# Optimization experiments

Measured on AMD Instinct MI355X. Metric: run time of the kernel, lower is better.

## Reference

```python
import jax, jax.numpy as jnp
import numpy as np

# -------- static config (mirrors init_kwargs / buffers at init) --------
B, S, H = 4, 2048, 1024
CTX, E, K = 64, 8, 2
POS_D = CTX // 2                 # 32
DG = H + CTX + POS_D             # 1120 actual gate-input width
HID = 3072                       # ByteMLP: 256*ceil(int(2*(4*DG)/3)/256)
N = B * S
# capacity = min(max(int(ceil(N*1.25/E) * mean(1/(clamp(0.5)+0.1))), 4), 2048)
CAPACITY = 2048
AUX_COEF = 0.01


def rmsnorm(x, w, eps=1e-6):
    return x * jax.lax.rsqrt(jnp.mean(x * x, axis=-1, keepdims=True) + eps) * w


def setup_inputs() -> dict:
    key = jax.random.key(0)
    ks = jax.random.split(key, 10)
    p = lambda k, shp: jax.random.normal(k, shp, jnp.float32) * 0.02
    return {
        "x": jax.random.normal(ks[0], (B, S, H), jnp.float32),
        "positions": jax.random.randint(ks[1], (B, S), 0, 4096, jnp.int32),
        "w_c1": p(ks[2], (H, 2 * H)), "b_c1": jnp.zeros((2 * H,), jnp.float32),
        "w_c2": p(ks[3], (2 * H, CTX)), "b_c2": jnp.zeros((CTX,), jnp.float32),
        "norm_w": jnp.ones((DG,), jnp.float32),
        "mlp_w1": p(ks[4], (DG, HID)),
        "mlp_w3": p(ks[5], (DG, HID)),
        "mlp_w2": p(ks[6], (HID, DG)),
        "proj_w": p(ks[7], (DG, E)),
        "pos_table": p(ks[8], (4096, POS_D)),
        "temperature": jnp.float32(1.0),
    }


def _gate(x, positions, w_c1, b_c1, w_c2, b_c2, norm_w, mlp_w1, mlp_w2, mlp_w3,
          proj_w, pos_table, temperature):
    x_flat = x.reshape(N, H)
    pos_emb = pos_table[positions.reshape(-1)]                       # [N,32]
    ctx = jax.nn.gelu(x_flat @ w_c1 + b_c1, approximate=False) @ w_c2 + b_c2
    context_feat = jnp.concatenate([ctx, pos_emb], axis=-1)          # [N,96]
    gi = jnp.concatenate([x_flat, context_feat], axis=-1)            # [N,DG]
    gi = rmsnorm(gi, norm_w)
    h = (jax.nn.silu(gi @ mlp_w1) * (gi @ mlp_w3)) @ mlp_w2          # SwiGLU MLP
    h = h + gi                                                       # residual
    logits = h @ proj_w                                              # [N,E]
    # expert_priority buffer == ones -> log prior is 0 (omitted)
    # expert_load buffer == zeros -> load_imbalance == 0 -> temp = temperature
    temp = jnp.maximum(temperature, 0.3)
    return jax.nn.softmax(logits / temp, axis=-1), context_feat


def reference(x, positions, w_c1, b_c1, w_c2, b_c2, norm_w, mlp_w1, mlp_w2,
              mlp_w3, proj_w, pos_table, temperature):
    scores, context_feat = _gate(x, positions, w_c1, b_c1, w_c2, b_c2, norm_w,
                                 mlp_w1, mlp_w2, mlp_w3, proj_w, pos_table,
                                 temperature)
    topk_scores, topk_idx = jax.lax.top_k(scores, K)                 # [N,K]

    # ---- vectorized greedy capacity dispatch (== torch per-token loop) ----
    fe = topk_idx.reshape(-1)                                        # [N*K]
    fw = topk_scores.reshape(-1)                                     # priority==1
    order = jnp.argsort(-fw)                                         # desc by weight
    e_sorted = fe[order]
    oh = jax.nn.one_hot(e_sorted, E, dtype=jnp.int32)                # [N*K,E]
    rank = jnp.take_along_axis(jnp.cumsum(oh, 0), e_sorted[:, None], 1)[:, 0] - 1
    ok = rank < CAPACITY
    slot_sorted = jnp.where(ok, rank, -1)
    NK = N * K
    slot = jnp.zeros((NK,), jnp.int32).at[order].set(slot_sorted.astype(jnp.int32))
    assigned = jnp.zeros((NK,), bool).at[order].set(ok)
    assigned_mask = assigned.reshape(N, K)
    buffer_positions = jnp.maximum(slot, 0).reshape(N, K)
    overflow_mask = ~assigned_mask.any(axis=-1)
    expert_count = jax.ops.segment_sum(assigned.astype(jnp.int32), fe,
                                       num_segments=E)

    # ---- load-balance aux loss (switch-style) ----
    me = scores.mean(axis=0)                                         # mean prob/expert
    ce = expert_count.astype(scores.dtype) / N                       # assigned frac
    aux_loss = AUX_COEF * E * jnp.sum(me * ce)

    next_context = context_feat.reshape(B, S, -1).mean(axis=1)       # [B,96]
    return (topk_idx, topk_scores, assigned_mask, buffer_positions,
            overflow_mask, expert_count, aux_loss, next_context)
```

## Files before the change

### kernel.cpp

```cpp
#include <hip/hip_runtime.h>
#include <math.h>

#define N_TOK 8192
#define HD    1024
#define CTXD  64
#define POS_D 32
#define DG    1120
#define HID   3072
#define NE    8
#define CAP   2048
#define NK    (N_TOK * 2)
#define CH    2048

typedef _Float16 half8 __attribute__((ext_vector_type(8)));
typedef float    floatx4 __attribute__((ext_vector_type(4)));

__device__ static inline void gl2lds16(const void* g, void* l) {
  __builtin_amdgcn_global_load_lds(
      (const __attribute__((address_space(1))) void*)g,
      (__attribute__((address_space(3))) void*)l, 16, 0, 0);
}

__global__ __launch_bounds__(256) void mfma_gemm(
    const _Float16* __restrict__ Ah, const _Float16* __restrict__ Al, int lda,
    const _Float16* __restrict__ Bh, const _Float16* __restrict__ Bl, int ldb,
    int Bn,
    const float* __restrict__ bias,
    float* __restrict__ Cf, _Float16* __restrict__ Oh, _Float16* __restrict__ Ol,
    int ldc,
    int Kd, int mode)
{
  __shared__ _Float16 smem[16384];
  _Float16* sAh = smem;
  _Float16* sAl = smem + 4096;
  _Float16* sBh = smem + 8192;
  _Float16* sBl = smem + 12288;

  const int tid = threadIdx.x;
  const int m0 = blockIdx.y * 128, n0 = blockIdx.x * 128;
  const int kbeg = blockIdx.z * Kd;

  const int q0 = tid, q1 = tid + 256;
  const int r0 = q0 >> 2, r1 = q1 >> 2;
  const int cg0 = (q0 & 3) ^ ((r0 >> 1) & 3);
  const int cg1 = (q1 & 3) ^ ((r1 >> 1) & 3);
  int br0 = n0 + r0; if (br0 >= Bn) br0 = Bn - 1;
  int br1 = n0 + r1; if (br1 >= Bn) br1 = Bn - 1;
  const _Float16* gA0h = Ah + (size_t)(m0 + r0) * lda + kbeg + cg0 * 8;
  const _Float16* gA1h = Ah + (size_t)(m0 + r1) * lda + kbeg + cg1 * 8;
  const _Float16* gA0l = Al + (size_t)(m0 + r0) * lda + kbeg + cg0 * 8;
  const _Float16* gA1l = Al + (size_t)(m0 + r1) * lda + kbeg + cg1 * 8;
  const _Float16* gB0h = Bh + (size_t)br0 * ldb + kbeg + cg0 * 8;
  const _Float16* gB1h = Bh + (size_t)br1 * ldb + kbeg + cg1 * 8;
  const _Float16* gB0l = Bl + (size_t)br0 * ldb + kbeg + cg0 * 8;
  const _Float16* gB1l = Bl + (size_t)br1 * ldb + kbeg + cg1 * 8;

  const int lane = tid & 63;
  const int wave = tid >> 6;
  const int wm = (wave >> 1) * 64, wn = (wave & 1) * 64;
  const int fr = lane & 15, quad = lane >> 4;
  int aoff[4], boff[4];
#pragma unroll
  for (int t = 0; t < 4; ++t) {
    int ar = wm + t * 16 + fr;
    aoff[t] = ar * 32 + (quad ^ ((ar >> 1) & 3)) * 8;
    int brr = wn + t * 16 + fr;
    boff[t] = brr * 32 + (quad ^ ((brr >> 1) & 3)) * 8;
  }

  floatx4 acc[4][4];
#pragma unroll
  for (int i = 0; i < 4; ++i)
#pragma unroll
    for (int j = 0; j < 4; ++j) {
      floatx4 z = {0.f, 0.f, 0.f, 0.f};
      acc[i][j] = z;
    }

  for (int k0 = 0; k0 < Kd; k0 += 32) {
    gl2lds16(gA0h, sAh + q0 * 8);
    gl2lds16(gA1h, sAh + q1 * 8);
    gl2lds16(gA0l, sAl + q0 * 8);
    gl2lds16(gA1l, sAl + q1 * 8);
    gl2lds16(gB0h, sBh + q0 * 8);
    gl2lds16(gB1h, sBh + q1 * 8);
    gl2lds16(gB0l, sBl + q0 * 8);
    gl2lds16(gB1l, sBl + q1 * 8);
    gA0h += 32; gA1h += 32; gA0l += 32; gA1l += 32;
    gB0h += 32; gB1h += 32; gB0l += 32; gB1l += 32;
    __syncthreads();

    half8 a_h[4], a_l[4], b_h[4], b_l[4];
#pragma unroll
    for (int t = 0; t < 4; ++t) {
      a_h[t] = *(const half8*)(sAh + aoff[t]);
      a_l[t] = *(const half8*)(sAl + aoff[t]);
      b_h[t] = *(const half8*)(sBh + boff[t]);
      b_l[t] = *(const half8*)(sBl + boff[t]);
    }
#pragma unroll
    for (int i = 0; i < 4; ++i)
#pragma unroll
      for (int j = 0; j < 4; ++j) {
        acc[i][j] = __builtin_amdgcn_mfma_f32_16x16x32_f16(a_h[i], b_h[j], acc[i][j], 0, 0, 0);
        acc[i][j] = __builtin_amdgcn_mfma_f32_16x16x32_f16(a_h[i], b_l[j], acc[i][j], 0, 0, 0);
        acc[i][j] = __builtin_amdgcn_mfma_f32_16x16x32_f16(a_l[i], b_h[j], acc[i][j], 0, 0, 0);
      }
    __syncthreads();
  }

#pragma unroll
  for (int j = 0; j < 4; ++j) {
    int col = n0 + wn + j * 16 + fr;
    if (col < Bn) {
      float bv = bias ? bias[col] : 0.f;
#pragma unroll
      for (int i = 0; i < 4; ++i) {
#pragma unroll
        for (int r = 0; r < 4; ++r) {
          int row = m0 + wm + i * 16 + quad * 4 + r;
          size_t idx = (size_t)row * ldc + col;
          float v = acc[i][j][r] + bv;
          if (mode == 1) {
            v = 0.5f * v * (1.0f + erff(v * 0.70710678118654752440f));
            _Float16 hh = (_Float16)v;
            Oh[idx] = hh; Ol[idx] = (_Float16)(v - (float)hh);
          } else if (mode == 5) {
            atomicAdd(&Cf[idx], v);
          } else {
            Cf[idx] = v;
          }
        }
      }
    }
  }
}

__global__ __launch_bounds__(256, 3) void mfma_swiglu64(
    const _Float16* __restrict__ Ah, const _Float16* __restrict__ Al, int lda,
    const _Float16* __restrict__ B1h, const _Float16* __restrict__ B1l,
    const _Float16* __restrict__ B2h, const _Float16* __restrict__ B2l, int ldb,
    _Float16* __restrict__ Oh, _Float16* __restrict__ Ol, int ldc,
    int Kd)
{
  __shared__ _Float16 smem[16384];
  _Float16* sAh  = smem;
  _Float16* sAl  = smem + 4096;
  _Float16* sB1h = smem + 8192;
  _Float16* sB1l = smem + 10240;
  _Float16* sB2h = smem + 12288;
  _Float16* sB2l = smem + 14336;

  const int tid = threadIdx.x;
  const int m0 = blockIdx.y * 128, n0 = blockIdx.x * 64;

  const int q0 = tid, q1 = tid + 256;
  const int ra0 = q0 >> 2, ra1 = q1 >> 2;
  const int ca0 = (q0 & 3) ^ ((ra0 >> 1) & 3);
  const int ca1 = (q1 & 3) ^ ((ra1 >> 1) & 3);
  const _Float16* gA0h = Ah + (size_t)(m0 + ra0) * lda + ca0 * 8;
  const _Float16* gA1h = Ah + (size_t)(m0 + ra1) * lda + ca1 * 8;
  const _Float16* gA0l = Al + (size_t)(m0 + ra0) * lda + ca0 * 8;
  const _Float16* gA1l = Al + (size_t)(m0 + ra1) * lda + ca1 * 8;
  const int rb = tid >> 2;
  const int cb = (tid & 3) ^ ((rb >> 1) & 3);
  const _Float16* gB1hp = B1h + (size_t)(n0 + rb) * ldb + cb * 8;
  const _Float16* gB1lp = B1l + (size_t)(n0 + rb) * ldb + cb * 8;
  const _Float16* gB2hp = B2h + (size_t)(n0 + rb) * ldb + cb * 8;
  const _Float16* gB2lp = B2l + (size_t)(n0 + rb) * ldb + cb * 8;

  const int lane = tid & 63;
  const int wave = tid >> 6;
  const int wm = (wave >> 1) * 64, wn = (wave & 1) * 32;
  const int fr = lane & 15, quad = lane >> 4;
  int aoff[4], boff[2];
#pragma unroll
  for (int t = 0; t < 4; ++t) {
    int ar = wm + t * 16 + fr;
    aoff[t] = ar * 32 + (quad ^ ((ar >> 1) & 3)) * 8;
  }
#pragma unroll
  for (int t = 0; t < 2; ++t) {
    int brr = wn + t * 16 + fr;
    boff[t] = brr * 32 + (quad ^ ((brr >> 1) & 3)) * 8;
  }

  floatx4 acc1[4][2], acc2[4][2];
#pragma unroll
  for (int i = 0; i < 4; ++i)
#pragma unroll
    for (int j = 0; j < 2; ++j) {
      floatx4 z = {0.f, 0.f, 0.f, 0.f};
      acc1[i][j] = z; acc2[i][j] = z;
    }

  for (int k0 = 0; k0 < Kd; k0 += 32) {
    gl2lds16(gA0h, sAh + q0 * 8);
    gl2lds16(gA1h, sAh + q1 * 8);
    gl2lds16(gA0l, sAl + q0 * 8);
    gl2lds16(gA1l, sAl + q1 * 8);
    gl2lds16(gB1hp, sB1h + tid * 8);
    gl2lds16(gB1lp, sB1l + tid * 8);
    gl2lds16(gB2hp, sB2h + tid * 8);
    gl2lds16(gB2lp, sB2l + tid * 8);
    gA0h += 32; gA1h += 32; gA0l += 32; gA1l += 32;
    gB1hp += 32; gB1lp += 32; gB2hp += 32; gB2lp += 32;
    __syncthreads();

    half8 a_h[4], a_l[4], b_h[2], b_l[2];
#pragma unroll
    for (int t = 0; t < 4; ++t) {
      a_h[t] = *(const half8*)(sAh + aoff[t]);
      a_l[t] = *(const half8*)(sAl + aoff[t]);
    }
#pragma unroll
    for (int t = 0; t < 2; ++t) {
      b_h[t] = *(const half8*)(sB1h + boff[t]);
      b_l[t] = *(const half8*)(sB1l + boff[t]);
    }
#pragma unroll
    for (int i = 0; i < 4; ++i)
#pragma unroll
      for (int j = 0; j < 2; ++j) {
        acc1[i][j] = __builtin_amdgcn_mfma_f32_16x16x32_f16(a_h[i], b_h[j], acc1[i][j], 0, 0, 0);
        acc1[i][j] = __builtin_amdgcn_mfma_f32_16x16x32_f16(a_h[i], b_l[j], acc1[i][j], 0, 0, 0);
        acc1[i][j] = __builtin_amdgcn_mfma_f32_16x16x32_f16(a_l[i], b_h[j], acc1[i][j], 0, 0, 0);
      }
#pragma unroll
    for (int t = 0; t < 2; ++t) {
      b_h[t] = *(const half8*)(sB2h + boff[t]);
      b_l[t] = *(const half8*)(sB2l + boff[t]);
    }
#pragma unroll
    for (int i = 0; i < 4; ++i)
#pragma unroll
      for (int j = 0; j < 2; ++j) {
        acc2[i][j] = __builtin_amdgcn_mfma_f32_16x16x32_f16(a_h[i], b_h[j], acc2[i][j], 0, 0, 0);
        acc2[i][j] = __builtin_amdgcn_mfma_f32_16x16x32_f16(a_h[i], b_l[j], acc2[i][j], 0, 0, 0);
        acc2[i][j] = __builtin_amdgcn_mfma_f32_16x16x32_f16(a_l[i], b_h[j], acc2[i][j], 0, 0, 0);
      }
    __syncthreads();
  }

#pragma unroll
  for (int j = 0; j < 2; ++j) {
    int col = n0 + wn + j * 16 + fr;
#pragma unroll
    for (int i = 0; i < 4; ++i) {
#pragma unroll
      for (int r = 0; r < 4; ++r) {
        int row = m0 + wm + i * 16 + quad * 4 + r;
        size_t idx = (size_t)row * ldc + col;
        float uu = acc1[i][j][r];
        float v = (uu / (1.0f + expf(-uu))) * acc2[i][j][r];
        _Float16 hh = (_Float16)v;
        Oh[idx] = hh; Ol[idx] = (_Float16)(v - (float)hh);
      }
    }
  }
}

__global__ void split_kernel(const float* __restrict__ src,
                             _Float16* __restrict__ h, _Float16* __restrict__ l, int n)
{
  int i = blockIdx.x * 256 + threadIdx.x;
  if (i < n) {
    float v = src[i];
    _Float16 hh = (_Float16)v;
    h[i] = hh;
    l[i] = (_Float16)(v - (float)hh);
  }
}

__global__ __launch_bounds__(256) void tsplit_kernel(
    const float* __restrict__ W, int K, int Nn,
    _Float16* __restrict__ Th, _Float16* __restrict__ Tl)
{
  __shared__ float tile[32][33];
  int k0 = blockIdx.x * 32, n0 = blockIdx.y * 32;
  int tx = threadIdx.x & 31, ty = threadIdx.x >> 5;
#pragma unroll
  for (int i = 0; i < 32; i += 8)
    tile[ty + i][tx] = W[(size_t)(k0 + ty + i) * Nn + (n0 + tx)];
  __syncthreads();
#pragma unroll
  for (int i = 0; i < 32; i += 8) {
    float v = tile[tx][ty + i];
    _Float16 hh = (_Float16)v;
    size_t idx = (size_t)(n0 + ty + i) * K + (k0 + tx);
    Th[idx] = hh;
    Tl[idx] = (_Float16)(v - (float)hh);
  }
}

__global__ void pwt_kernel(const float* __restrict__ pw, float* __restrict__ pwt)
{
  int idx = blockIdx.x * 256 + threadIdx.x;
  if (idx < DG * NE) {
    int e = idx / DG, c = idx % DG;
    pwt[idx] = pw[c * NE + e];
  }
}

__global__ void gi_bias_init_kernel(float* __restrict__ gi, const float* __restrict__ b)
{
  int idx = blockIdx.x * 256 + threadIdx.x;
  if (idx < N_TOK * 64) {
    int row = idx >> 6, col = idx & 63;
    gi[(size_t)row * DG + 1024 + col] = b[col];
  }
}

__global__ void copy_x_kernel(const float* __restrict__ x, float* __restrict__ gi)
{
  int idx = blockIdx.x * 256 + threadIdx.x;
  if (idx < N_TOK * (HD / 4)) {
    int row = idx >> 8;
    int c4  = idx & 255;
    ((float4*)gi)[(size_t)row * (DG / 4) + c4] = ((const float4*)x)[idx];
  }
}

__global__ void pos_kernel(const int* __restrict__ positions,
                           const float* __restrict__ pt, float* __restrict__ gi)
{
  int idx = blockIdx.x * 256 + threadIdx.x;
  if (idx < N_TOK * (POS_D / 4)) {
    int row = idx >> 3;
    int j4  = idx & 7;
    ((float4*)gi)[(size_t)row * (DG / 4) + (1088 / 4) + j4] =
        ((const float4*)pt)[(size_t)positions[row] * 8 + j4];
  }
}

__global__ __launch_bounds__(256) void nctx_kernel(const float* __restrict__ gi,
                                                   float* __restrict__ o_nc)
{
  int b = blockIdx.x / 96, c = blockIdx.x % 96;
  int t = threadIdx.x;
  float s = 0.f;
  for (int srow = t; srow < 2048; srow += 256)
    s += gi[(size_t)(b * 2048 + srow) * DG + 1024 + c];
  for (int off = 32; off; off >>= 1) s += __shfl_xor(s, off, 64);
  __shared__ float red[4];
  if ((t & 63) == 0) red[t >> 6] = s;
  __syncthreads();
  if (t == 0) o_nc[b * 96 + c] = (red[0] + red[1] + red[2] + red[3]) * (1.f / 2048.f);
}

__global__ __launch_bounds__(256) void rmsnorm_kernel(float* __restrict__ gi,
                                                      const float* __restrict__ w,
                                                      _Float16* __restrict__ gih,
                                                      _Float16* __restrict__ gil)
{
  int row = blockIdx.x, t = threadIdx.x;
  float* g = gi + (size_t)row * DG;
  float s = 0.f;
  for (int c = t; c < DG; c += 256) { float v = g[c]; s += v * v; }
  for (int off = 32; off; off >>= 1) s += __shfl_xor(s, off, 64);
  __shared__ float red[4];
  if ((t & 63) == 0) red[t >> 6] = s;
  __syncthreads();
  float tot = red[0] + red[1] + red[2] + red[3];
  float scale = rsqrtf(tot * (1.0f / DG) + 1e-6f);
  for (int c = t; c < DG; c += 256) {
    float v = g[c] * scale * w[c];
    g[c] = v;
    _Float16 hh = (_Float16)v;
    size_t idx = (size_t)row * DG + c;
    gih[idx] = hh;
    gil[idx] = (_Float16)(v - (float)hh);
  }
}

__global__ __launch_bounds__(64) void logits_kernel(
    const float* __restrict__ h, const float* __restrict__ pwt,
    const float* __restrict__ tptr,
    float* __restrict__ scores, float* __restrict__ o_idx,
    float* __restrict__ o_val, unsigned long long* __restrict__ keys,
    int* __restrict__ fe)
{
  const int row = blockIdx.x;
  const int lane = threadIdx.x;
  const float* hr = h + (size_t)row * DG;

  float acc[NE];
#pragma unroll
  for (int e = 0; e < NE; ++e) acc[e] = 0.f;

#pragma unroll
  for (int it = 0; it < 4; ++it) {
    int c = it * 256 + lane * 4;
    float4 hv = *(const float4*)(hr + c);
#pragma unroll
    for (int e = 0; e < NE; ++e) {
      float4 wv = *(const float4*)(pwt + e * DG + c);
      acc[e] += hv.x * wv.x + hv.y * wv.y + hv.z * wv.z + hv.w * wv.w;
    }
  }
  if (lane < 24) {
    int c = 1024 + lane * 4;
    float4 hv = *(const float4*)(hr + c);
#pragma unroll
    for (int e = 0; e < NE; ++e) {
      float4 wv = *(const float4*)(pwt + e * DG + c);
      acc[e] += hv.x * wv.x + hv.y * wv.y + hv.z * wv.z + hv.w * wv.w;
    }
  }
#pragma unroll
  for (int e = 0; e < NE; ++e)
    for (int off = 32; off; off >>= 1) acc[e] += __shfl_xor(acc[e], off, 64);

  if (lane == 0) {
    float temp = fmaxf(tptr[0], 0.3f);
    float l[NE];
    float mx = -1e30f;
#pragma unroll
    for (int e = 0; e < NE; ++e) { l[e] = acc[e] / temp; mx = fmaxf(mx, l[e]); }
    float s = 0.f;
#pragma unroll
    for (int e = 0; e < NE; ++e) { l[e] = expf(l[e] - mx); s += l[e]; }
    float inv = 1.f / s;
#pragma unroll
    for (int e = 0; e < NE; ++e) { l[e] *= inv; scores[(size_t)row * NE + e] = l[e]; }
    int i0 = 0;
#pragma unroll
    for (int e = 1; e < NE; ++e) if (l[e] > l[i0]) i0 = e;
    int i1 = -1;
#pragma unroll
    for (int e = 0; e < NE; ++e)
      if (e != i0 && (i1 < 0 || l[e] > l[i1])) i1 = e;
    o_idx[row * 2 + 0] = (float)i0;  o_idx[row * 2 + 1] = (float)i1;
    o_val[row * 2 + 0] = l[i0];      o_val[row * 2 + 1] = l[i1];
    fe[row * 2 + 0] = i0;     fe[row * 2 + 1] = i1;
    unsigned int wb0 = __float_as_uint(l[i0]);
    unsigned int wb1 = __float_as_uint(l[i1]);
    keys[row * 2 + 0] = ((unsigned long long)i0 << 45) |
                        ((unsigned long long)wb0 << 14) |
                        (unsigned long long)(16383 - (row * 2 + 0));
    keys[row * 2 + 1] = ((unsigned long long)i1 << 45) |
                        ((unsigned long long)wb1 << 14) |
                        (unsigned long long)(16383 - (row * 2 + 1));
  }
}

__global__ __launch_bounds__(256) void hist_kernel(
    const int* __restrict__ fe, unsigned int* __restrict__ hist)
{
  __shared__ unsigned int lh[NE];
  if (threadIdx.x < NE) lh[threadIdx.x] = 0;
  __syncthreads();
  for (int i = blockIdx.x * 256 + threadIdx.x; i < NK; i += gridDim.x * 256)
    atomicAdd(&lh[fe[i]], 1u);
  __syncthreads();
  if (threadIdx.x < NE) atomicAdd(&hist[threadIdx.x], lh[threadIdx.x]);
}

__global__ void zero_small_kernel(int* __restrict__ ecnt, unsigned int* __restrict__ hist)
{
  if (threadIdx.x < NE) { ecnt[threadIdx.x] = 0; hist[threadIdx.x] = 0; }
}

__global__ void zero_gcnt_kernel(int* __restrict__ gcnt)
{
  int i = blockIdx.x * 256 + threadIdx.x;
  if (i < NK) gcnt[i] = 0;
}

__global__ __launch_bounds__(256) void rank_partial_kernel(
    const unsigned long long* __restrict__ keys, int* __restrict__ gcnt)
{
  __shared__ unsigned long long sk[1024];
  int i = blockIdx.x * 256 + threadIdx.x;
  unsigned long long ki = keys[i];
  int base = blockIdx.y * 1024;
  for (int j = threadIdx.x; j < 1024; j += 256)
    sk[j] = keys[base + j];
  __syncthreads();
  int c = 0;
#pragma unroll 8
  for (int jj = 0; jj < 1024; ++jj)
    c += (sk[jj] > ki) ? 1 : 0;
  atomicAdd(&gcnt[i], c);
}

__global__ __launch_bounds__(256) void rank_finalize_kernel(
    const int* __restrict__ gcnt, const int* __restrict__ fe,
    const unsigned int* __restrict__ hist,
    float* __restrict__ o_asg, float* __restrict__ o_pos, int* __restrict__ ecnt)
{
  int i = blockIdx.x * 256 + threadIdx.x;
  if (i >= NK) return;
  int e = fe[i];
  int suf = 0;
#pragma unroll
  for (int e2 = 0; e2 < NE; ++e2) suf += (e2 > e) ? (int)hist[e2] : 0;
  int rank = gcnt[i] - suf;
  bool assigned = rank < CAP;
  o_asg[i] = assigned ? 1.f : 0.f;
  o_pos[i] = assigned ? (float)rank : 0.f;
  if (assigned) atomicAdd(&ecnt[e], 1);
}

__global__ void overflow_kernel(const float* __restrict__ o_asg, float* __restrict__ o_ovf)
{
  int n = blockIdx.x * 256 + threadIdx.x;
  if (n < N_TOK)
    o_ovf[n] = (o_asg[n * 2] + o_asg[n * 2 + 1] > 0.f) ? 0.f : 1.f;
}

__global__ __launch_bounds__(256) void me_kernel(const float* __restrict__ scores,
                                                 float* __restrict__ me_sum)
{
  int e = blockIdx.x, t = threadIdx.x;
  float s = 0.f;
  for (int r = t; r < N_TOK; r += 256) s += scores[(size_t)r * NE + e];
  for (int off = 32; off; off >>= 1) s += __shfl_xor(s, off, 64);
  __shared__ float red[4];
  if ((t & 63) == 0) red[t >> 6] = s;
  __syncthreads();
  if (t == 0) me_sum[e] = red[0] + red[1] + red[2] + red[3];
}

__global__ void finalize_kernel(const int* __restrict__ ecnt,
                                const float* __restrict__ me_sum,
                                float* __restrict__ o_ec, float* __restrict__ o_aux)
{
  if (threadIdx.x == 0) {
    float aux = 0.f;
    for (int e = 0; e < NE; ++e) {
      float ce = (float)ecnt[e] * (1.f / N_TOK);
      float me = me_sum[e] * (1.f / N_TOK);
      aux += me * ce;
      o_ec[e] = (float)ecnt[e];
    }
    o_aux[0] = 0.01f * 8.f * aux;
  }
}

extern "C" void kernel_launch(void* const* d_in, const int* in_sizes, int n_in,
                              void* d_out, int out_size, void* d_ws, size_t ws_size,
                              hipStream_t stream)
{
  (void)in_sizes; (void)n_in; (void)out_size; (void)ws_size;
  const float* x         = (const float*)d_in[0];
  const int*   positions = (const int*)d_in[1];
  const float* w_c1      = (const float*)d_in[2];
  const float* b_c1      = (const float*)d_in[3];
  const float* w_c2      = (const float*)d_in[4];
  const float* b_c2      = (const float*)d_in[5];
  const float* norm_w    = (const float*)d_in[6];
  const float* mlp_w1    = (const float*)d_in[7];
  const float* mlp_w3    = (const float*)d_in[8];
  const float* mlp_w2    = (const float*)d_in[9];
  const float* proj_w    = (const float*)d_in[10];
  const float* pos_table = (const float*)d_in[11];
  const float* temperature = (const float*)d_in[12];

  float* out   = (float*)d_out;
  float* o_idx = out;
  float* o_val = out + 16384;
  float* o_asg = out + 32768;
  float* o_pos = out + 49152;
  float* o_ovf = out + 65536;
  float* o_ec  = out + 73728;
  float* o_aux = out + 73736;
  float* o_nc  = out + 73737;

  char* p = (char*)d_ws;
  auto take = [&](size_t bytes) { char* r = p; p += (bytes + 255) & ~(size_t)255; return r; };

  float*    gi  = (float*)take((size_t)N_TOK * DG * 4);
  _Float16* gih = (_Float16*)take((size_t)N_TOK * DG * 2);
  _Float16* gil = (_Float16*)take((size_t)N_TOK * DG * 2);

  _Float16* WR = (_Float16*)take((size_t)6 * DG * HID * 2);
  _Float16* wc1th = WR;
  _Float16* wc1tl = WR + 2097152;
  _Float16* wc2th = WR + 4194304;
  _Float16* wc2tl = WR + 4325376;
  _Float16* w1th  = WR;
  _Float16* w1tl  = WR + 3440640;
  _Float16* w3th  = WR + 6881280;
  _Float16* w3tl  = WR + 10321920;
  _Float16* w2th  = WR + 13762560;
  _Float16* w2tl  = WR + 17203200;

  char* CR = take((size_t)50331648);
  _Float16* xh   = (_Float16*)CR;
  _Float16* xl   = (_Float16*)(CR + 8388608);
  _Float16* ctxh = (_Float16*)(CR + 16777216);
  _Float16* ctxl = (_Float16*)(CR + 33554432);
  _Float16* Xh   = (_Float16*)CR;
  _Float16* Xl   = (_Float16*)(CR + 25165824);

  float* scores = (float*)take((size_t)N_TOK * NE * 4);
  unsigned long long* keys = (unsigned long long*)take((size_t)NK * 8);
  int*   fe     = (int*)take((size_t)NK * 4);
  int*   gcnt   = (int*)take((size_t)NK * 4);
  float* pwt    = (float*)take((size_t)DG * NE * 4);
  int*   ecnt   = (int*)take(256);
  unsigned int* hist = (unsigned int*)take(256);
  float* me_sum = (float*)take(256);

  gi_bias_init_kernel<<<(N_TOK * 64 + 255) / 256, 256, 0, stream>>>(gi, b_c2);
  copy_x_kernel<<<(N_TOK * (HD / 4) + 255) / 256, 256, 0, stream>>>(x, gi);
  pos_kernel<<<(N_TOK * (POS_D / 4) + 255) / 256, 256, 0, stream>>>(positions, pos_table, gi);

  tsplit_kernel<<<dim3(HD / 32, CH / 32),   256, 0, stream>>>(w_c1, HD, CH, wc1th, wc1tl);
  tsplit_kernel<<<dim3(CH / 32, CTXD / 32), 256, 0, stream>>>(w_c2, CH, CTXD, wc2th, wc2tl);
  for (int c = 0; c < 2; ++c) {
    size_t base = (size_t)c * 4096;
    split_kernel<<<(4096 * HD + 255) / 256, 256, 0, stream>>>(
        x + base * HD, xh, xl, 4096 * HD);
    mfma_gemm<<<dim3(CH / 128, 4096 / 128), 256, 0, stream>>>(
        xh, xl, HD, wc1th, wc1tl, HD, CH, b_c1,
        nullptr, ctxh, ctxl, CH, HD, 1);
    mfma_gemm<<<dim3(1, 4096 / 128, 8), 256, 0, stream>>>(
        ctxh, ctxl, CH, wc2th, wc2tl, CH, CTXD, nullptr,
        gi + base * DG + 1024, nullptr, nullptr, DG, CH / 8, 5);
  }

  nctx_kernel<<<4 * 96, 256, 0, stream>>>(gi, o_nc);
  rmsnorm_kernel<<<N_TOK, 256, 0, stream>>>(gi, norm_w, gih, gil);

  tsplit_kernel<<<dim3(DG / 32, HID / 32), 256, 0, stream>>>(mlp_w1, DG, HID, w1th, w1tl);
  tsplit_kernel<<<dim3(DG / 32, HID / 32), 256, 0, stream>>>(mlp_w3, DG, HID, w3th, w3tl);
  tsplit_kernel<<<dim3(HID / 32, DG / 32), 256, 0, stream>>>(mlp_w2, HID, DG, w2th, w2tl);
  for (int c = 0; c < 2; ++c) {
    size_t base = (size_t)c * 4096;
    const _Float16* ah = gih + base * DG;
    const _Float16* al = gil + base * DG;
    mfma_swiglu64<<<dim3(HID / 64, 4096 / 128), 256, 0, stream>>>(
        ah, al, DG, w1th, w1tl, w3th, w3tl, DG, Xh, Xl, HID, DG);
    mfma_gemm<<<dim3((DG + 127) / 128, 4096 / 128, 3), 256, 0, stream>>>(
        Xh, Xl, HID, w2th, w2tl, HID, DG, nullptr,
        gi + base * DG, nullptr, nullptr, DG, HID / 3, 5);
  }

  pwt_kernel<<<(DG * NE + 255) / 256, 256, 0, stream>>>(proj_w, pwt);
  zero_small_kernel<<<1, 64, 0, stream>>>(ecnt, hist);
  zero_gcnt_kernel<<<NK / 256, 256, 0, stream>>>(gcnt);
  logits_kernel<<<N_TOK, 64, 0, stream>>>(gi, pwt, temperature,
                                          scores, o_idx, o_val, keys, fe);
  hist_kernel<<<16, 256, 0, stream>>>(fe, hist);
  rank_partial_kernel<<<dim3(NK / 256, NK / 1024), 256, 0, stream>>>(keys, gcnt);
  rank_finalize_kernel<<<NK / 256, 256, 0, stream>>>(gcnt, fe, hist, o_asg, o_pos, ecnt);
  overflow_kernel<<<N_TOK / 256, 256, 0, stream>>>(o_asg, o_ovf);
  me_kernel<<<NE, 256, 0, stream>>>(scores, me_sum);
  finalize_kernel<<<1, 64, 0, stream>>>(ecnt, me_sum, o_ec, o_aux);
}
```

Before: 1.099 ms.

## Use 32x32x16 MFMA in SwiGLU GEMM and merge small setup kernels

The fused SwiGLU up-projection kernel now uses 32x32x16 f16 MFMA tiles with floatx16 accumulators instead of 16x16x32, which cuts the number of LDS fragment loads per MFMA and issues fewer, larger matrix instructions. The epilogue row mapping is rewritten to match the 32x32 output layout. Separately, the bias-init and position-embedding kernels are merged into one, and the proj-weight transpose is merged with the zeroing kernels, removing several launches. The larger accumulators raise register pressure, and the 32x32 fragment layout could change LDS bank behaviour.

Measured after the change: 1.153 ms. 1.05x slower.

```diff
diff --git a/kernel.cpp b/kernel.cpp
--- a/kernel.cpp
+++ b/kernel.cpp
@@ -14,6 +14,7 @@
 
 typedef _Float16 half8 __attribute__((ext_vector_type(8)));
 typedef float    floatx4 __attribute__((ext_vector_type(4)));
+typedef float    floatx16 __attribute__((ext_vector_type(16)));
 
 __device__ static inline void gl2lds16(const void* g, void* l) {
   __builtin_amdgcn_global_load_lds(
@@ -172,27 +173,29 @@
   const int lane = tid & 63;
   const int wave = tid >> 6;
   const int wm = (wave >> 1) * 64, wn = (wave & 1) * 32;
-  const int fr = lane & 15, quad = lane >> 4;
-  int aoff[4], boff[2];
-#pragma unroll
-  for (int t = 0; t < 4; ++t) {
-    int ar = wm + t * 16 + fr;
-    aoff[t] = ar * 32 + (quad ^ ((ar >> 1) & 3)) * 8;
-  }
+  const int l31 = lane & 31, g = lane >> 5;
+  int aoff[2][2], boff[2];
 #pragma unroll
   for (int t = 0; t < 2; ++t) {
-    int brr = wn + t * 16 + fr;
-    boff[t] = brr * 32 + (quad ^ ((brr >> 1) & 3)) * 8;
-  }
-
-  floatx4 acc1[4][2], acc2[4][2];
-#pragma unroll
-  for (int i = 0; i < 4; ++i)
-#pragma unroll
-    for (int j = 0; j < 2; ++j) {
-      floatx4 z = {0.f, 0.f, 0.f, 0.f};
-      acc1[i][j] = z; acc2[i][j] = z;
-    }
+    int ar = wm + t * 32 + l31;
+#pragma unroll
+    for (int s = 0; s < 2; ++s) {
+      int chunk = s * 2 + g;
+      aoff[t][s] = ar * 32 + (chunk ^ ((ar >> 1) & 3)) * 8;
+    }
+  }
+  {
+    int brr = wn + l31;
+#pragma unroll
+    for (int s = 0; s < 2; ++s)
+      boff[s] = brr * 32 + ((s * 2 + g) ^ ((brr >> 1) & 3)) * 8;
+  }
+
+  floatx16 acc1[2], acc2[2];
+#pragma unroll
+  for (int t = 0; t < 2; ++t)
+#pragma unroll
+    for (int r = 0; r < 16; ++r) { acc1[t][r] = 0.f; acc2[t][r] = 0.f; }
 
   for (int k0 = 0; k0 < Kd; k0 += 32) {
     gl2lds16(gA0h, sAh + q0 * 8);
@@ -207,55 +210,46 @@
     gB1hp += 32; gB1lp += 32; gB2hp += 32; gB2lp += 32;
     __syncthreads();
 
-    half8 a_h[4], a_l[4], b_h[2], b_l[2];
-#pragma unroll
-    for (int t = 0; t < 4; ++t) {
-      a_h[t] = *(const half8*)(sAh + aoff[t]);
-      a_l[t] = *(const half8*)(sAl + aoff[t]);
-    }
-#pragma unroll
-    for (int t = 0; t < 2; ++t) {
-      b_h[t] = *(const half8*)(sB1h + boff[t]);
-      b_l[t] = *(const half8*)(sB1l + boff[t]);
-    }
-#pragma unroll
-    for (int i = 0; i < 4; ++i)
-#pragma unroll
-      for (int j = 0; j < 2; ++j) {
-        acc1[i][j] = __builtin_amdgcn_mfma_f32_16x16x32_f16(a_h[i], b_h[j], acc1[i][j], 0, 0, 0);
-        acc1[i][j] = __builtin_amdgcn_mfma_f32_16x16x32_f16(a_h[i], b_l[j], acc1[i][j], 0, 0, 0);
-        acc1[i][j] = __builtin_amdgcn_mfma_f32_16x16x32_f16(a_l[i], b_h[j], acc1[i][j], 0, 0, 0);
+    half8 a_h[2][2], a_l[2][2], b1h[2], b1l[2], b2h[2], b2l[2];
+#pragma unroll
+    for (int t = 0; t < 2; ++t)
+#pragma unroll
+      for (int s = 0; s < 2; ++s) {
+        a_h[t][s] = *(const half8*)(sAh + aoff[t][s]);
+        a_l[t][s] = *(const half8*)(sAl + aoff[t][s]);
       }
 #pragma unroll
-    for (int t = 0; t < 2; ++t) {
-      b_h[t] = *(const half8*)(sB2h + boff[t]);
-      b_l[t] = *(const half8*)(sB2l + boff[t]);
-    }
-#pragma unroll
-    for (int i = 0; i < 4; ++i)
-#pragma unroll
-      for (int j = 0; j < 2; ++j) {
-        acc2[i][j] = __builtin_amdgcn_mfma_f32_16x16x32_f16(a_h[i], b_h[j], acc2[i][j], 0, 0, 0);
-        acc2[i][j] = __builtin_amdgcn_mfma_f32_16x16x32_f16(a_h[i], b_l[j], acc2[i][j], 0, 0, 0);
-        acc2[i][j] = __builtin_amdgcn_mfma_f32_16x16x32_f16(a_l[i], b_h[j], acc2[i][j], 0, 0, 0);
+    for (int s = 0; s < 2; ++s) {
+      b1h[s] = *(const half8*)(sB1h + boff[s]);
+      b1l[s] = *(const half8*)(sB1l + boff[s]);
+      b2h[s] = *(const half8*)(sB2h + boff[s]);
+      b2l[s] = *(const half8*)(sB2l + boff[s]);
+    }
+#pragma unroll
+    for (int t = 0; t < 2; ++t)
+#pragma unroll
+      for (int s = 0; s < 2; ++s) {
+        acc1[t] = __builtin_amdgcn_mfma_f32_32x32x16_f16(a_h[t][s], b1h[s], acc1[t], 0, 0, 0);
+        acc1[t] = __builtin_amdgcn_mfma_f32_32x32x16_f16(a_h[t][s], b1l[s], acc1[t], 0, 0, 0);
+        acc1[t] = __builtin_amdgcn_mfma_f32_32x32x16_f16(a_l[t][s], b1h[s], acc1[t], 0, 0, 0);
+        acc2[t] = __builtin_amdgcn_mfma_f32_32x32x16_f16(a_h[t][s], b2h[s], acc2[t], 0, 0, 0);
+        acc2[t] = __builtin_amdgcn_mfma_f32_32x32x16_f16(a_h[t][s], b2l[s], acc2[t], 0, 0, 0);
+        acc2[t] = __builtin_amdgcn_mfma_f32_32x32x16_f16(a_l[t][s], b2h[s], acc2[t], 0, 0, 0);
       }
     __syncthreads();
   }
 
-#pragma unroll
-  for (int j = 0; j < 2; ++j) {
-    int col = n0 + wn + j * 16 + fr;
-#pragma unroll
-    for (int i = 0; i < 4; ++i) {
-#pragma unroll
-      for (int r = 0; r < 4; ++r) {
-        int row = m0 + wm + i * 16 + quad * 4 + r;
-        size_t idx = (size_t)row * ldc + col;
-        float uu = acc1[i][j][r];
-        float v = (uu / (1.0f + expf(-uu))) * acc2[i][j][r];
-        _Float16 hh = (_Float16)v;
-        Oh[idx] = hh; Ol[idx] = (_Float16)(v - (float)hh);
-      }
+  const int col = n0 + wn + l31;
+#pragma unroll
+  for (int t = 0; t < 2; ++t) {
+#pragma unroll
+    for (int r = 0; r < 16; ++r) {
+      int row = m0 + wm + t * 32 + (r & 3) + 8 * (r >> 2) + 4 * g;
+      size_t idx = (size_t)row * ldc + col;
+      float uu = acc1[t][r];
+      float v = (uu / (1.0f + expf(-uu))) * acc2[t][r];
+      _Float16 hh = (_Float16)v;
+      Oh[idx] = hh; Ol[idx] = (_Float16)(v - (float)hh);
     }
   }
 }
@@ -293,21 +287,21 @@
   }
 }
 
-__global__ void pwt_kernel(const float* __restrict__ pw, float* __restrict__ pwt)
-{
-  int idx = blockIdx.x * 256 + threadIdx.x;
-  if (idx < DG * NE) {
-    int e = idx / DG, c = idx % DG;
-    pwt[idx] = pw[c * NE + e];
-  }
-}
-
-__global__ void gi_bias_init_kernel(float* __restrict__ gi, const float* __restrict__ b)
+__global__ void gi_misc_kernel(const float* __restrict__ b,
+                               const int* __restrict__ positions,
+                               const float* __restrict__ pt,
+                               float* __restrict__ gi)
 {
   int idx = blockIdx.x * 256 + threadIdx.x;
   if (idx < N_TOK * 64) {
     int row = idx >> 6, col = idx & 63;
     gi[(size_t)row * DG + 1024 + col] = b[col];
+  }
+  if (idx < N_TOK * (POS_D / 4)) {
+    int row = idx >> 3;
+    int j4  = idx & 7;
+    ((float4*)gi)[(size_t)row * (DG / 4) + (1088 / 4) + j4] =
+        ((const float4*)pt)[(size_t)positions[row] * 8 + j4];
   }
 }
 
@@ -318,18 +312,6 @@
     int row = idx >> 8;
     int c4  = idx & 255;
     ((float4*)gi)[(size_t)row * (DG / 4) + c4] = ((const float4*)x)[idx];
-  }
-}
-
-__global__ void pos_kernel(const int* __restrict__ positions,
-                           const float* __restrict__ pt, float* __restrict__ gi)
-{
-  int idx = blockIdx.x * 256 + threadIdx.x;
-  if (idx < N_TOK * (POS_D / 4)) {
-    int row = idx >> 3;
-    int j4  = idx & 7;
-    ((float4*)gi)[(size_t)row * (DG / 4) + (1088 / 4) + j4] =
-        ((const float4*)pt)[(size_t)positions[row] * 8 + j4];
   }
 }
 
@@ -456,15 +438,14 @@
   if (threadIdx.x < NE) atomicAdd(&hist[threadIdx.x], lh[threadIdx.x]);
 }
 
-__global__ void zero_small_kernel(int* __restrict__ ecnt, unsigned int* __restrict__ hist)
-{
-  if (threadIdx.x < NE) { ecnt[threadIdx.x] = 0; hist[threadIdx.x] = 0; }
-}
-
-__global__ void zero_gcnt_kernel(int* __restrict__ gcnt)
+__global__ void router_prep_kernel(const float* __restrict__ pw, float* __restrict__ pwt,
+                                   int* __restrict__ ecnt, unsigned int* __restrict__ hist,
+                                   int* __restrict__ gcnt)
 {
   int i = blockIdx.x * 256 + threadIdx.x;
   if (i < NK) gcnt[i] = 0;
+  if (i < DG * NE) { int e = i / DG, c = i % DG; pwt[i] = pw[c * NE + e]; }
+  if (i < NE) { ecnt[i] = 0; hist[i] = 0; }
 }
 
 __global__ __launch_bounds__(256) void rank_partial_kernel(
@@ -603,9 +584,8 @@
   unsigned int* hist = (unsigned int*)take(256);
   float* me_sum = (float*)take(256);
 
-  gi_bias_init_kernel<<<(N_TOK * 64 + 255) / 256, 256, 0, stream>>>(gi, b_c2);
   copy_x_kernel<<<(N_TOK * (HD / 4) + 255) / 256, 256, 0, stream>>>(x, gi);
-  pos_kernel<<<(N_TOK * (POS_D / 4) + 255) / 256, 256, 0, stream>>>(positions, pos_table, gi);
+  gi_misc_kernel<<<(N_TOK * 64 + 255) / 256, 256, 0, stream>>>(b_c2, positions, pos_table, gi);
 
   tsplit_kernel<<<dim3(HD / 32, CH / 32),   256, 0, stream>>>(w_c1, HD, CH, wc1th, wc1tl);
   tsplit_kernel<<<dim3(CH / 32, CTXD / 32), 256, 0, stream>>>(w_c2, CH, CTXD, wc2th, wc2tl);
@@ -638,9 +618,7 @@
         gi + base * DG, nullptr, nullptr, DG, HID / 3, 5);
   }
 
-  pwt_kernel<<<(DG * NE + 255) / 256, 256, 0, stream>>>(proj_w, pwt);
-  zero_small_kernel<<<1, 64, 0, stream>>>(ecnt, hist);
-  zero_gcnt_kernel<<<NK / 256, 256, 0, stream>>>(gcnt);
+  router_prep_kernel<<<NK / 256, 256, 0, stream>>>(proj_w, pwt, ecnt, hist, gcnt);
   logits_kernel<<<N_TOK, 64, 0, stream>>>(gi, pwt, temperature,
                                           scores, o_idx, o_val, keys, fe);
   hist_kernel<<<16, 256, 0, stream>>>(fe, hist);
```
